# Performance work log

Measured on AMD Instinct MI355X. Metric: run time of the kernel, lower is better.

The kernel has to match this reference:

```python
import jax, jax.numpy as jnp
import numpy as np

SLOPE = 25.0   # fast_sigmoid surrogate slope
THR = 1.0      # snntorch Leaky default threshold


@jax.custom_vjp
def spike(x):
    # Heaviside forward, fast-sigmoid surrogate backward
    return (x > 0).astype(x.dtype)

def _spike_fwd(x):
    return spike(x), x

def _spike_bwd(x, g):
    return (g / (SLOPE * jnp.abs(x) + 1.0) ** 2,)

spike.defvjp(_spike_fwd, _spike_bwd)


def conv2d(x, w, b):
    y = jax.lax.conv_general_dilated(
        x, w, window_strides=(1, 1), padding=((1, 1), (1, 1)),
        dimension_numbers=('NCHW', 'OIHW', 'NCHW'))
    return y + b[None, :, None, None]


def maxpool2(x):
    return jax.lax.reduce_window(x, -jnp.inf, jax.lax.max,
                                 (1, 1, 2, 2), (1, 1, 2, 2), 'VALID')


def bn_inf(x, g, b, m, v):
    # inference-mode BatchNorm2d, eps = 1e-5
    inv = g * jax.lax.rsqrt(v + 1e-5)
    return x * inv[None, :, None, None] + (b - m * inv)[None, :, None, None]


def lif_step(mem, inp, beta):
    # snntorch Leaky, reset_mechanism='subtract', learn_beta (clamped to [0,1])
    b = jnp.clip(beta, 0.0, 1.0)
    reset = jax.lax.stop_gradient((mem > THR).astype(mem.dtype))
    mem_new = b * mem + inp - reset * THR
    spk = spike(mem_new - THR)
    return spk, mem_new


def setup_inputs() -> dict:
    key = jax.random.key(0)
    ks = jax.random.split(key, 20)
    T, B, H, W = 25, 512, 100, 64   # T steps, batch, MAX_LEN, N_MELS
    NUM_CLASSES = 35
    FLAT = 32 * (H // 4) * (W // 4)  # 12800
    f32 = jnp.float32
    inp = {
        'x': jax.random.normal(ks[0], (T, B, H, W), f32),
        'conv1_w': jax.random.normal(ks[1], (16, 1, 3, 3), f32) * 0.2,
        'conv1_b': jnp.zeros((16,), f32),
        'bn1_g': jnp.ones((16,), f32),
        'bn1_b': jnp.zeros((16,), f32),
        'bn1_m': jax.random.normal(ks[2], (16,), f32) * 0.1,
        'bn1_v': jax.random.uniform(ks[3], (16,), f32) + 0.5,
        'conv2_w': jax.random.normal(ks[4], (32, 16, 3, 3), f32) * (1.0 / np.sqrt(16 * 9)),
        'conv2_b': jnp.zeros((32,), f32),
        'bn2_g': jnp.ones((32,), f32),
        'bn2_b': jnp.zeros((32,), f32),
        'bn2_m': jax.random.normal(ks[5], (32,), f32) * 0.1,
        'bn2_v': jax.random.uniform(ks[6], (32,), f32) + 0.5,
        'fc1_w': jax.random.normal(ks[7], (256, FLAT), f32) * (1.0 / np.sqrt(FLAT)),
        'fc1_b': jnp.zeros((256,), f32),
        'fc2_w': jax.random.normal(ks[8], (128, 256), f32) * (1.0 / np.sqrt(256)),
        'fc2_b': jnp.zeros((128,), f32),
        'fc3_w': jax.random.normal(ks[9], (NUM_CLASSES, 128), f32) * (1.0 / np.sqrt(128)),
        'fc3_b': jnp.zeros((NUM_CLASSES,), f32),
        'beta1': jnp.float32(0.9),
        'beta2': jnp.float32(0.9),
        'beta3': jnp.float32(0.9),
    }
    return inp


def reference(x, conv1_w, conv1_b, bn1_g, bn1_b, bn1_m, bn1_v,
              conv2_w, conv2_b, bn2_g, bn2_b, bn2_m, bn2_v,
              fc1_w, fc1_b, fc2_w, fc2_b, fc3_w, fc3_b,
              beta1, beta2, beta3):
    T, B = x.shape[0], x.shape[1]
    # CNN runs once on the time-averaged input
    x_mean = jnp.mean(x, axis=0)[:, None]          # (B, 1, H, W)
    f = maxpool2(jax.nn.relu(bn_inf(conv2d(x_mean, conv1_w, conv1_b), bn1_g, bn1_b, bn1_m, bn1_v)))
    f = maxpool2(jax.nn.relu(bn_inf(conv2d(f, conv2_w, conv2_b), bn2_g, bn2_b, bn2_m, bn2_v)))
    feat = f.reshape(B, -1)                        # (B, FLAT)
    # fc1 input is the same every step (dropout = identity in eval)
    cur1 = feat @ fc1_w.T + fc1_b                  # (B, 256)

    m1 = jnp.zeros((B, fc1_w.shape[0]), x.dtype)
    m2 = jnp.zeros((B, fc2_w.shape[0]), x.dtype)
    m3 = jnp.zeros((B, fc3_w.shape[0]), x.dtype)

    def step(carry, _):
        m1, m2, m3 = carry
        spk1, m1 = lif_step(m1, cur1, beta1)
        spk2, m2 = lif_step(m2, spk1 @ fc2_w.T + fc2_b, beta2)
        spk3, m3 = lif_step(m3, spk2 @ fc3_w.T + fc3_b, beta3)
        return (m1, m2, m3), spk3

    _, out = jax.lax.scan(step, (m1, m2, m3), None, length=T)
    return out                                     # (T, B, NUM_CLASSES)
```

## Files before the change

### kernel.cpp

```cpp
#include <hip/hip_runtime.h>

typedef float f4nt __attribute__((ext_vector_type(4)));

#define WS_P1    0
#define WS_FEAT  13107200
#define WS_PART  0
#define WS_S1    8388608
#define WS_IN2   11665408
#define WS_S2    13303808
#define WS_IN3   14942208
#define WS_WL    19660800
#define WS_SH2   (WS_WL + 4608)

__global__ void prep_kernel(const float* __restrict__ w2, const float* __restrict__ cb2,
                            const float* __restrict__ g2, const float* __restrict__ bb2,
                            const float* __restrict__ m2, const float* __restrict__ v2,
                            float* __restrict__ wlg, float* __restrict__ sh2g) {
    const int tid = threadIdx.x;
    for (int i = tid; i < 4608; i += 256) {
        int c = i / 144, rem = i - c * 144;
        float inv = g2[c] * rsqrtf(v2[c] + 1e-5f);
        wlg[rem * 32 + c] = w2[i] * inv;
    }
    if (tid < 32) {
        float inv = g2[tid] * rsqrtf(v2[tid] + 1e-5f);
        sh2g[tid] = cb2[tid] * inv + bb2[tid] - m2[tid] * inv;
    }
}

__global__ __launch_bounds__(384) void conv1_kernel(const float* __restrict__ x,
                                                    const float* __restrict__ w1,
                                                    const float* __restrict__ cb1,
                                                    const float* __restrict__ g1,
                                                    const float* __restrict__ bb1,
                                                    const float* __restrict__ m1g,
                                                    const float* __restrict__ v1,
                                                    float* __restrict__ p1) {
    __shared__ float xs[22 * 66];
    __shared__ float w1s[144];
    __shared__ float sh1s[16];
    const int b = blockIdx.x, s = blockIdx.y;
    const int tid = threadIdx.x;
    if (tid < 144) {
        int c = tid / 9;
        float inv = g1[c] * rsqrtf(v1[c] + 1e-5f);
        w1s[tid] = w1[tid] * inv;
    }
    if (tid >= 144 && tid < 160) {
        int c = tid - 144;
        float inv = g1[c] * rsqrtf(v1[c] + 1e-5f);
        sh1s[c] = cb1[c] * inv + bb1[c] - m1g[c] * inv;
    }
    if (tid >= 160 && tid < 204) {
        int q = tid - 160;
        xs[(q >> 1) * 66 + (q & 1) * 65] = 0.f;
    }
    const int r0 = s * 20 - 1;
    const size_t TSTR = (size_t)512 * 6400;
    if (tid < 352) {
        int lr = tid >> 4, cq = tid & 15;
        int gr = r0 + lr;
        f4nt a0 = {0.f, 0.f, 0.f, 0.f}, a1 = a0, a2 = a0, a3 = a0;
        if (gr >= 0 && gr < 100) {
            const float* px = x + (size_t)b * 6400 + gr * 64 + cq * 4;
            #pragma unroll
            for (int tt = 0; tt < 24; tt += 4) {
                f4nt v0 = __builtin_nontemporal_load((const f4nt*)(px + (size_t)(tt + 0) * TSTR));
                f4nt v1_ = __builtin_nontemporal_load((const f4nt*)(px + (size_t)(tt + 1) * TSTR));
                f4nt v2_ = __builtin_nontemporal_load((const f4nt*)(px + (size_t)(tt + 2) * TSTR));
                f4nt v3 = __builtin_nontemporal_load((const f4nt*)(px + (size_t)(tt + 3) * TSTR));
                a0 += v0; a1 += v1_; a2 += v2_; a3 += v3;
            }
            f4nt v = __builtin_nontemporal_load((const f4nt*)(px + (size_t)24 * TSTR));
            a0 += v;
        }
        const float sc = 1.0f / 25.0f;
        f4nt sm = (a0 + a1 + a2 + a3) * sc;
        float* d = &xs[lr * 66 + 1 + cq * 4];
        d[0] = sm.x; d[1] = sm.y; d[2] = sm.z; d[3] = sm.w;
    }
    __syncthreads();
    if (tid < 320) {
        int phl = tid >> 5, pw = tid & 31;
        int ph = s * 10 + phl;
        float win[4][4];
        #pragma unroll
        for (int a = 0; a < 4; ++a)
            #pragma unroll
            for (int c2 = 0; c2 < 4; ++c2)
                win[a][c2] = xs[(2 * phl + a) * 66 + 2 * pw + c2];
        #pragma unroll 1
        for (int c = 0; c < 16; ++c) {
            float s00 = 0.f, s01 = 0.f, s10 = 0.f, s11 = 0.f;
            #pragma unroll
            for (int dh = 0; dh < 3; ++dh)
                #pragma unroll
                for (int dw = 0; dw < 3; ++dw) {
                    float w = w1s[c * 9 + dh * 3 + dw];
                    s00 = fmaf(win[dh][dw],         w, s00);
                    s01 = fmaf(win[dh][dw + 1],     w, s01);
                    s10 = fmaf(win[dh + 1][dw],     w, s10);
                    s11 = fmaf(win[dh + 1][dw + 1], w, s11);
                }
            float m = fmaxf(fmaxf(s00, s01), fmaxf(s10, s11));
            float val = fmaxf(m + sh1s[c], 0.f);
            p1[(((size_t)b * 50 + ph) * 16 + c) * 32 + pw] = val;
        }
    }
}

__global__ __launch_bounds__(256) void conv2_kernel(const float* __restrict__ p1,
                                                    const float* __restrict__ wlg,
                                                    const float* __restrict__ sh2g,
                                                    float* __restrict__ feat) {
    __shared__ __align__(16) float ins[10 * 16 * 36];
    const int s = blockIdx.x, b = blockIdx.y;
    const int tid = threadIdx.x;
    const int chg = tid & 15, q = (tid >> 4) & 3, phl = tid >> 6;
    const int ph = s * 4 + phl;
    const int xb = q * 8;
    const float* wbase = wlg + 2 * chg;

    float2 wcur[9], wnxt[9];
    #pragma unroll
    for (int t = 0; t < 9; ++t)
        wcur[t] = *(const float2*)&wbase[t * 32];
    if (tid < 160) {
        int lr = tid >> 4, ci = tid & 15;
        int gr = s * 8 - 1 + lr;
        float* dst = &ins[(lr * 16 + ci) * 36];
        if (gr >= 0 && gr < 50) {
            const float* src = p1 + (((size_t)b * 50 + gr) * 16 + ci) * 32;
            float4 v0 = *(const float4*)src;
            dst[0] = 0.f; dst[1] = v0.x; dst[2] = v0.y; dst[3] = v0.z;
            #pragma unroll
            for (int qq = 1; qq < 8; ++qq) {
                float4 v = *(const float4*)(src + 4 * qq - 1);
                *(float4*)(dst + 4 * qq) = v;
            }
            dst[32] = src[31];
            dst[33] = 0.f; dst[34] = 0.f; dst[35] = 0.f;
        } else {
            #pragma unroll
            for (int qq = 0; qq < 9; ++qq) *(float4*)(dst + 4 * qq) = make_float4(0.f, 0.f, 0.f, 0.f);
        }
    }
    __syncthreads();

    float acc[2][2][8];
    #pragma unroll
    for (int c = 0; c < 2; ++c)
        #pragma unroll
        for (int a = 0; a < 2; ++a)
            #pragma unroll
            for (int xx = 0; xx < 8; ++xx) acc[c][a][xx] = 0.f;

    #pragma unroll 1
    for (int ci = 0; ci < 16; ++ci) {
        if (ci < 15) {
            #pragma unroll
            for (int t = 0; t < 9; ++t)
                wnxt[t] = *(const float2*)&wbase[((ci + 1) * 9 + t) * 32];
        }
        #pragma unroll
        for (int lr4 = 0; lr4 < 4; ++lr4) {
            const float* row = &ins[((2 * phl + lr4) * 16 + ci) * 36 + xb];
            float v[10];
            float4 t0 = *(const float4*)&row[0];
            float4 t1 = *(const float4*)&row[4];
            float2 t2 = *(const float2*)&row[8];
            v[0]=t0.x; v[1]=t0.y; v[2]=t0.z; v[3]=t0.w;
            v[4]=t1.x; v[5]=t1.y; v[6]=t1.z; v[7]=t1.w;
            v[8]=t2.x; v[9]=t2.y;
            #pragma unroll
            for (int a = 0; a < 2; ++a) {
                const int dh = lr4 - a;
                if (dh >= 0 && dh <= 2) {
                    #pragma unroll
                    for (int dw = 0; dw < 3; ++dw) {
                        float w0 = wcur[dh * 3 + dw].x;
                        float w1 = wcur[dh * 3 + dw].y;
                        #pragma unroll
                        for (int xx = 0; xx < 8; ++xx) {
                            acc[0][a][xx] = fmaf(v[xx + dw], w0, acc[0][a][xx]);
                            acc[1][a][xx] = fmaf(v[xx + dw], w1, acc[1][a][xx]);
                        }
                    }
                }
            }
        }
        #pragma unroll
        for (int t = 0; t < 9; ++t) wcur[t] = wnxt[t];
    }
    if (ph < 25) {
        #pragma unroll
        for (int ch = 0; ch < 2; ++ch) {
            const int c = 2 * chg + ch;
            const float sh = sh2g[c];
            #pragma unroll
            for (int p = 0; p < 4; ++p) {
                float m = fmaxf(fmaxf(acc[ch][0][2 * p], acc[ch][0][2 * p + 1]),
                                fmaxf(acc[ch][1][2 * p], acc[ch][1][2 * p + 1]));
                float val = fmaxf(m + sh, 0.f);
                feat[(((size_t)b * 32 + c) * 25 + ph) * 16 + q * 4 + p] = val;
            }
        }
    }
}

__global__ __launch_bounds__(256, 1) void fc1_kernel(const float* __restrict__ feat,
                                                     const float* __restrict__ w,
                                                     float* __restrict__ part) {
    __shared__ float As[8 * 136];
    __shared__ float Bs[8 * 320];
    const int bx = blockIdx.x, bz = blockIdx.y;
    const int tid = threadIdx.x;
    const int tm = tid >> 5, tn = tid & 31;
    const int m0 = bx * 128;
    const int k0 = bz * 200;
    const int ar = tid >> 1, ac4 = (tid & 1) * 4;
    const int br = tid >> 1, bh = (tid & 1) * 4;
    const int gb0 = (br >> 3) * 10 + (br & 7);
    const int gb1 = ((br + 128) >> 3) * 10 + (br & 7);

    float acc[16][8] = {};
    float4 aP  = *(const float4*)(feat + (size_t)(m0 + ar) * 12800 + k0 + ac4);
    float4 bP0 = *(const float4*)(w + (size_t)br * 12800 + k0 + bh);
    float4 bP1 = *(const float4*)(w + (size_t)(br + 128) * 12800 + k0 + bh);

    for (int st = 0; st < 25; ++st) {
        __syncthreads();
        As[(ac4 + 0) * 136 + ar] = aP.x; As[(ac4 + 1) * 136 + ar] = aP.y;
        As[(ac4 + 2) * 136 + ar] = aP.z; As[(ac4 + 3) * 136 + ar] = aP.w;
        Bs[(bh + 0) * 320 + gb0] = bP0.x; Bs[(bh + 1) * 320 + gb0] = bP0.y;
        Bs[(bh + 2) * 320 + gb0] = bP0.z; Bs[(bh + 3) * 320 + gb0] = bP0.w;
        Bs[(bh + 0) * 320 + gb1] = bP1.x; Bs[(bh + 1) * 320 + gb1] = bP1.y;
        Bs[(bh + 2) * 320 + gb1] = bP1.z; Bs[(bh + 3) * 320 + gb1] = bP1.w;
        __syncthreads();
        if (st < 24) {
            const int o = k0 + (st + 1) * 8;
            aP  = *(const float4*)(feat + (size_t)(m0 + ar) * 12800 + o + ac4);
            bP0 = *(const float4*)(w + (size_t)br * 12800 + o + bh);
            bP1 = *(const float4*)(w + (size_t)(br + 128) * 12800 + o + bh);
        }
        #pragma unroll
        for (int kk = 0; kk < 8; ++kk) {
            float4 a0 = *(const float4*)&As[kk * 136 + tm * 16];
            float4 a1 = *(const float4*)&As[kk * 136 + tm * 16 + 4];
            float4 a2 = *(const float4*)&As[kk * 136 + tm * 16 + 8];
            float4 a3 = *(const float4*)&As[kk * 136 + tm * 16 + 12];
            float4 b0 = *(const float4*)&Bs[kk * 320 + tn * 10];
            float4 b1 = *(const float4*)&Bs[kk * 320 + tn * 10 + 4];
            float a_[16] = {a0.x, a0.y, a0.z, a0.w, a1.x, a1.y, a1.z, a1.w,
                            a2.x, a2.y, a2.z, a2.w, a3.x, a3.y, a3.z, a3.w};
            float b_[8]  = {b0.x, b0.y, b0.z, b0.w, b1.x, b1.y, b1.z, b1.w};
            #pragma unroll
            for (int i = 0; i < 16; ++i)
                #pragma unroll
                for (int j = 0; j < 8; ++j)
                    acc[i][j] = fmaf(a_[i], b_[j], acc[i][j]);
        }
    }
    #pragma unroll
    for (int i = 0; i < 16; ++i) {
        float* dst = &part[(size_t)bz * 131072 + (size_t)(m0 + tm * 16 + i) * 256 + tn * 8];
        *(float4*)dst       = make_float4(acc[i][0], acc[i][1], acc[i][2], acc[i][3]);
        *(float4*)(dst + 4) = make_float4(acc[i][4], acc[i][5], acc[i][6], acc[i][7]);
    }
}

__global__ __launch_bounds__(256) void lif1_kernel(const float* __restrict__ part,
                                                   const float* __restrict__ b1g,
                                                   const float* __restrict__ pb1,
                                                   float* __restrict__ S1) {
    const int i = blockIdx.x * 256 + threadIdx.x;
    const int k = i & 255;
    float cu = b1g[k];
    #pragma unroll 8
    for (int z = 0; z < 64; ++z) cu += part[(size_t)z * 131072 + i];
    const float be = fminf(fmaxf(pb1[0], 0.f), 1.f);
    float m = 0.f;
    #pragma unroll
    for (int t = 0; t < 25; ++t) {
        float r = (m > 1.f) ? 1.f : 0.f;
        m = fmaf(be, m, cu) - r;
        S1[(size_t)t * 131072 + i] = (m > 1.f) ? 1.f : 0.f;
    }
}

__global__ __launch_bounds__(256) void fc2g_kernel(const float* __restrict__ S1,
                                                   const float* __restrict__ w2g,
                                                   const float* __restrict__ b2g,
                                                   float* __restrict__ in2) {
    __shared__ float As[16 * 36];
    __shared__ float Bs[16 * 136];
    const int m0 = blockIdx.x * 32;
    const int tid = threadIdx.x;
    const int tm = tid >> 4, tn = tid & 15;
    const int ra = tid >> 2, cqa = tid & 3;
    const int rb = tid >> 1, kb = (tid & 1) * 8;
    float acc[2][8] = {};
    float4 av = make_float4(0.f, 0.f, 0.f, 0.f);
    if (tid < 128) av = *(const float4*)&S1[(size_t)(m0 + ra) * 256 + cqa * 4];
    float4 bv0 = *(const float4*)&w2g[rb * 256 + kb];
    float4 bv1 = *(const float4*)&w2g[rb * 256 + kb + 4];

    for (int kt = 0; kt < 16; ++kt) {
        __syncthreads();
        if (tid < 128) {
            As[(cqa * 4 + 0) * 36 + ra] = av.x; As[(cqa * 4 + 1) * 36 + ra] = av.y;
            As[(cqa * 4 + 2) * 36 + ra] = av.z; As[(cqa * 4 + 3) * 36 + ra] = av.w;
        }
        Bs[(kb + 0) * 136 + rb] = bv0.x; Bs[(kb + 1) * 136 + rb] = bv0.y;
        Bs[(kb + 2) * 136 + rb] = bv0.z; Bs[(kb + 3) * 136 + rb] = bv0.w;
        Bs[(kb + 4) * 136 + rb] = bv1.x; Bs[(kb + 5) * 136 + rb] = bv1.y;
        Bs[(kb + 6) * 136 + rb] = bv1.z; Bs[(kb + 7) * 136 + rb] = bv1.w;
        __syncthreads();
        if (kt < 15) {
            const int o = (kt + 1) * 16;
            if (tid < 128) av = *(const float4*)&S1[(size_t)(m0 + ra) * 256 + o + cqa * 4];
            bv0 = *(const float4*)&w2g[rb * 256 + o + kb];
            bv1 = *(const float4*)&w2g[rb * 256 + o + kb + 4];
        }
        #pragma unroll
        for (int kk = 0; kk < 16; ++kk) {
            float2 a2 = *(const float2*)&As[kk * 36 + tm * 2];
            float4 bw0 = *(const float4*)&Bs[kk * 136 + tn * 8];
            float4 bw1 = *(const float4*)&Bs[kk * 136 + tn * 8 + 4];
            float b_[8] = {bw0.x, bw0.y, bw0.z, bw0.w, bw1.x, bw1.y, bw1.z, bw1.w};
            #pragma unroll
            for (int j = 0; j < 8; ++j) {
                acc[0][j] = fmaf(a2.x, b_[j], acc[0][j]);
                acc[1][j] = fmaf(a2.y, b_[j], acc[1][j]);
            }
        }
    }
    float4 bb0 = *(const float4*)&b2g[tn * 8];
    float4 bb1 = *(const float4*)&b2g[tn * 8 + 4];
    #pragma unroll
    for (int i = 0; i < 2; ++i) {
        float* dst = &in2[(size_t)(m0 + tm * 2 + i) * 128 + tn * 8];
        *(float4*)dst       = make_float4(acc[i][0] + bb0.x, acc[i][1] + bb0.y,
                                          acc[i][2] + bb0.z, acc[i][3] + bb0.w);
        *(float4*)(dst + 4) = make_float4(acc[i][4] + bb1.x, acc[i][5] + bb1.y,
                                          acc[i][6] + bb1.z, acc[i][7] + bb1.w);
    }
}

__global__ __launch_bounds__(256) void lif2_kernel(const float* __restrict__ in2,
                                                   const float* __restrict__ pb2,
                                                   float* __restrict__ S2) {
    const int i = blockIdx.x * 256 + threadIdx.x;
    const float be = fminf(fmaxf(pb2[0], 0.f), 1.f);
    float m = 0.f;
    #pragma unroll
    for (int t = 0; t < 25; ++t) {
        float r = (m > 1.f) ? 1.f : 0.f;
        m = fmaf(be, m, in2[(size_t)t * 65536 + i]) - r;
        S2[(size_t)t * 65536 + i] = (m > 1.f) ? 1.f : 0.f;
    }
}

__global__ __launch_bounds__(256) void fc3g_kernel(const float* __restrict__ S2,
                                                   const float* __restrict__ w3g,
                                                   const float* __restrict__ b3g,
                                                   float* __restrict__ in3) {
    __shared__ float As[16 * 36];
    __shared__ float Bs[16 * 48];
    const int m0 = blockIdx.x * 32;
    const int tid = threadIdx.x;
    const int tm = tid >> 4, tn = tid & 15;
    float acc[2][3] = {};
    for (int kt = 0; kt < 8; ++kt) {
        __syncthreads();
        if (tid < 128) {
            int r = tid >> 2, cq = tid & 3;
            float4 av = *(const float4*)&S2[(size_t)(m0 + r) * 128 + kt * 16 + cq * 4];
            As[(cq * 4 + 0) * 36 + r] = av.x; As[(cq * 4 + 1) * 36 + r] = av.y;
            As[(cq * 4 + 2) * 36 + r] = av.z; As[(cq * 4 + 3) * 36 + r] = av.w;
        }
        for (int i = tid; i < 560; i += 256) {
            int kk = i / 35, c = i - kk * 35;
            Bs[kk * 48 + c] = w3g[c * 128 + kt * 16 + kk];
        }
        __syncthreads();
        #pragma unroll
        for (int kk = 0; kk < 16; ++kk) {
            float2 a2 = *(const float2*)&As[kk * 36 + tm * 2];
            float w0 = Bs[kk * 48 + tn];
            float w1 = Bs[kk * 48 + tn + 16];
            float w2 = Bs[kk * 48 + tn + 32];
            acc[0][0] = fmaf(a2.x, w0, acc[0][0]); acc[1][0] = fmaf(a2.y, w0, acc[1][0]);
            acc[0][1] = fmaf(a2.x, w1, acc[0][1]); acc[1][1] = fmaf(a2.y, w1, acc[1][1]);
            acc[0][2] = fmaf(a2.x, w2, acc[0][2]); acc[1][2] = fmaf(a2.y, w2, acc[1][2]);
        }
    }
    const float bias0 = b3g[tn];
    const float bias1 = b3g[tn + 16];
    const float bias2 = (tn < 3) ? b3g[tn + 32] : 0.f;
    #pragma unroll
    for (int i = 0; i < 2; ++i) {
        const size_t row = (size_t)(m0 + tm * 2 + i) * 35;
        in3[row + tn]      = acc[i][0] + bias0;
        in3[row + tn + 16] = acc[i][1] + bias1;
        if (tn < 3) in3[row + tn + 32] = acc[i][2] + bias2;
    }
}

__global__ __launch_bounds__(256) void lif3_kernel(const float* __restrict__ in3,
                                                   const float* __restrict__ pb3,
                                                   float* __restrict__ out) {
    const int i = blockIdx.x * 256 + threadIdx.x;
    if (i >= 17920) return;
    const float be = fminf(fmaxf(pb3[0], 0.f), 1.f);
    float m = 0.f;
    #pragma unroll
    for (int t = 0; t < 25; ++t) {
        float r = (m > 1.f) ? 1.f : 0.f;
        m = fmaf(be, m, in3[(size_t)t * 17920 + i]) - r;
        out[(size_t)t * 17920 + i] = (m > 1.f) ? 1.f : 0.f;
    }
}

extern "C" void kernel_launch(void* const* d_in, const int* in_sizes, int n_in,
                              void* d_out, int out_size, void* d_ws, size_t ws_size,
                              hipStream_t stream) {
    const float* x     = (const float*)d_in[0];
    const float* c1w   = (const float*)d_in[1];
    const float* c1b   = (const float*)d_in[2];
    const float* bn1g  = (const float*)d_in[3];
    const float* bn1b  = (const float*)d_in[4];
    const float* bn1m  = (const float*)d_in[5];
    const float* bn1v  = (const float*)d_in[6];
    const float* c2w   = (const float*)d_in[7];
    const float* c2b   = (const float*)d_in[8];
    const float* bn2g  = (const float*)d_in[9];
    const float* bn2b  = (const float*)d_in[10];
    const float* bn2m  = (const float*)d_in[11];
    const float* bn2v  = (const float*)d_in[12];
    const float* fc1w  = (const float*)d_in[13];
    const float* fc1b  = (const float*)d_in[14];
    const float* fc2w  = (const float*)d_in[15];
    const float* fc2b  = (const float*)d_in[16];
    const float* fc3w  = (const float*)d_in[17];
    const float* fc3b  = (const float*)d_in[18];
    const float* beta1 = (const float*)d_in[19];
    const float* beta2 = (const float*)d_in[20];
    const float* beta3 = (const float*)d_in[21];
    float* ws  = (float*)d_ws;
    float* out = (float*)d_out;

    prep_kernel<<<1, 256, 0, stream>>>(c2w, c2b, bn2g, bn2b, bn2m, bn2v,
                                       ws + WS_WL, ws + WS_SH2);
    conv1_kernel<<<dim3(512, 5), 384, 0, stream>>>(x, c1w, c1b, bn1g, bn1b, bn1m, bn1v,
                                                   ws + WS_P1);
    conv2_kernel<<<dim3(7, 512), 256, 0, stream>>>(ws + WS_P1, ws + WS_WL, ws + WS_SH2,
                                                   ws + WS_FEAT);
    fc1_kernel<<<dim3(4, 64), 256, 0, stream>>>(ws + WS_FEAT, fc1w, ws + WS_PART);
    lif1_kernel<<<512, 256, 0, stream>>>(ws + WS_PART, fc1b, beta1, ws + WS_S1);
    fc2g_kernel<<<400, 256, 0, stream>>>(ws + WS_S1, fc2w, fc2b, ws + WS_IN2);
    lif2_kernel<<<256, 256, 0, stream>>>(ws + WS_IN2, beta2, ws + WS_S2);
    fc3g_kernel<<<400, 256, 0, stream>>>(ws + WS_S2, fc3w, fc3b, ws + WS_IN3);
    lif3_kernel<<<70, 256, 0, stream>>>(ws + WS_IN3, beta3, out);
}
```

Measured before the change: 299.3 us.

## Fuse conv1 and conv2 into one kernel keeping pooled conv1 output in LDS

Merges the conv1+BN+ReLU+pool stage with the conv2 stage so the intermediate pooled map stays in shared memory instead of going through global memory. Each block now recomputes conv1 for its halo rows, reading 22 input rows across all 25 timesteps per 8-row output tile. This removes the intermediate write/read and one launch, but increases redundant reads of the large time-series input due to halo overlap.

```diff
diff --git a/kernel.cpp b/kernel.cpp
--- a/kernel.cpp
+++ b/kernel.cpp
@@ -2,7 +2,6 @@
 
 typedef float f4nt __attribute__((ext_vector_type(4)));
 
-#define WS_P1    0
 #define WS_FEAT  13107200
 #define WS_PART  0
 #define WS_S1    8388608
@@ -28,19 +27,23 @@
     }
 }
 
-__global__ __launch_bounds__(384) void conv1_kernel(const float* __restrict__ x,
-                                                    const float* __restrict__ w1,
-                                                    const float* __restrict__ cb1,
-                                                    const float* __restrict__ g1,
-                                                    const float* __restrict__ bb1,
-                                                    const float* __restrict__ m1g,
-                                                    const float* __restrict__ v1,
-                                                    float* __restrict__ p1) {
+__global__ __launch_bounds__(256) void fused_conv_kernel(const float* __restrict__ x,
+                                                         const float* __restrict__ w1,
+                                                         const float* __restrict__ cb1,
+                                                         const float* __restrict__ g1,
+                                                         const float* __restrict__ bb1,
+                                                         const float* __restrict__ m1g,
+                                                         const float* __restrict__ v1,
+                                                         const float* __restrict__ wlg,
+                                                         const float* __restrict__ sh2g,
+                                                         float* __restrict__ feat) {
     __shared__ float xs[22 * 66];
+    __shared__ __align__(16) float p1L[10 * 16 * 36];
     __shared__ float w1s[144];
     __shared__ float sh1s[16];
-    const int b = blockIdx.x, s = blockIdx.y;
+    const int s = blockIdx.x, b = blockIdx.y;
     const int tid = threadIdx.x;
+
     if (tid < 144) {
         int c = tid / 9;
         float inv = g1[c] * rsqrtf(v1[c] + 1e-5f);
@@ -51,102 +54,84 @@
         float inv = g1[c] * rsqrtf(v1[c] + 1e-5f);
         sh1s[c] = cb1[c] * inv + bb1[c] - m1g[c] * inv;
     }
-    if (tid >= 160 && tid < 204) {
-        int q = tid - 160;
+
+    const size_t TSTR = (size_t)512 * 6400;
+    if (tid < 176) {
+        int lr = tid >> 3, cq = tid & 7;
+        int gxr = 16 * s - 3 + lr;
+        f4nt a0 = {0.f, 0.f, 0.f, 0.f}, a1 = a0, c0 = a0, c1 = a0;
+        if (gxr >= 0 && gxr < 100) {
+            const float* px = x + (size_t)b * 6400 + gxr * 64 + cq * 8;
+            #pragma unroll
+            for (int tt = 0; tt < 24; tt += 2) {
+                f4nt u0 = __builtin_nontemporal_load((const f4nt*)(px + (size_t)tt * TSTR));
+                f4nt u1 = __builtin_nontemporal_load((const f4nt*)(px + (size_t)tt * TSTR + 4));
+                f4nt u2 = __builtin_nontemporal_load((const f4nt*)(px + (size_t)(tt + 1) * TSTR));
+                f4nt u3 = __builtin_nontemporal_load((const f4nt*)(px + (size_t)(tt + 1) * TSTR + 4));
+                a0 += u0; a1 += u1; c0 += u2; c1 += u3;
+            }
+            f4nt u0 = __builtin_nontemporal_load((const f4nt*)(px + (size_t)24 * TSTR));
+            f4nt u1 = __builtin_nontemporal_load((const f4nt*)(px + (size_t)24 * TSTR + 4));
+            a0 += u0; a1 += u1;
+            a0 += c0; a1 += c1;
+            a0 *= (1.0f / 25.0f); a1 *= (1.0f / 25.0f);
+        }
+        float* d = &xs[lr * 66 + 1 + cq * 8];
+        d[0] = a0.x; d[1] = a0.y; d[2] = a0.z; d[3] = a0.w;
+        d[4] = a1.x; d[5] = a1.y; d[6] = a1.z; d[7] = a1.w;
+    } else if (tid < 220) {
+        int q = tid - 176;
         xs[(q >> 1) * 66 + (q & 1) * 65] = 0.f;
     }
-    const int r0 = s * 20 - 1;
-    const size_t TSTR = (size_t)512 * 6400;
-    if (tid < 352) {
-        int lr = tid >> 4, cq = tid & 15;
-        int gr = r0 + lr;
-        f4nt a0 = {0.f, 0.f, 0.f, 0.f}, a1 = a0, a2 = a0, a3 = a0;
-        if (gr >= 0 && gr < 100) {
-            const float* px = x + (size_t)b * 6400 + gr * 64 + cq * 4;
-            #pragma unroll
-            for (int tt = 0; tt < 24; tt += 4) {
-                f4nt v0 = __builtin_nontemporal_load((const f4nt*)(px + (size_t)(tt + 0) * TSTR));
-                f4nt v1_ = __builtin_nontemporal_load((const f4nt*)(px + (size_t)(tt + 1) * TSTR));
-                f4nt v2_ = __builtin_nontemporal_load((const f4nt*)(px + (size_t)(tt + 2) * TSTR));
-                f4nt v3 = __builtin_nontemporal_load((const f4nt*)(px + (size_t)(tt + 3) * TSTR));
-                a0 += v0; a1 += v1_; a2 += v2_; a3 += v3;
+    __syncthreads();
+
+    #pragma unroll 1
+    for (int pos = tid; pos < 320; pos += 256) {
+        int j = pos >> 5, pw = pos & 31;
+        int gr = s * 8 - 1 + j;
+        if (gr >= 0 && gr < 50) {
+            float win[4][4];
+            #pragma unroll
+            for (int a = 0; a < 4; ++a)
+                #pragma unroll
+                for (int cc = 0; cc < 4; ++cc)
+                    win[a][cc] = xs[(2 * j + a) * 66 + 2 * pw + cc];
+            #pragma unroll 1
+            for (int c = 0; c < 16; ++c) {
+                float s00 = 0.f, s01 = 0.f, s10 = 0.f, s11 = 0.f;
+                #pragma unroll
+                for (int dh = 0; dh < 3; ++dh)
+                    #pragma unroll
+                    for (int dw = 0; dw < 3; ++dw) {
+                        float w = w1s[c * 9 + dh * 3 + dw];
+                        s00 = fmaf(win[dh][dw],         w, s00);
+                        s01 = fmaf(win[dh][dw + 1],     w, s01);
+                        s10 = fmaf(win[dh + 1][dw],     w, s10);
+                        s11 = fmaf(win[dh + 1][dw + 1], w, s11);
+                    }
+                float m = fmaxf(fmaxf(s00, s01), fmaxf(s10, s11));
+                p1L[(j * 16 + c) * 36 + 1 + pw] = fmaxf(m + sh1s[c], 0.f);
             }
-            f4nt v = __builtin_nontemporal_load((const f4nt*)(px + (size_t)24 * TSTR));
-            a0 += v;
-        }
-        const float sc = 1.0f / 25.0f;
-        f4nt sm = (a0 + a1 + a2 + a3) * sc;
-        float* d = &xs[lr * 66 + 1 + cq * 4];
-        d[0] = sm.x; d[1] = sm.y; d[2] = sm.z; d[3] = sm.w;
-    }
-    __syncthreads();
-    if (tid < 320) {
-        int phl = tid >> 5, pw = tid & 31;
-        int ph = s * 10 + phl;
-        float win[4][4];
-        #pragma unroll
-        for (int a = 0; a < 4; ++a)
-            #pragma unroll
-            for (int c2 = 0; c2 < 4; ++c2)
-                win[a][c2] = xs[(2 * phl + a) * 66 + 2 * pw + c2];
-        #pragma unroll 1
-        for (int c = 0; c < 16; ++c) {
-            float s00 = 0.f, s01 = 0.f, s10 = 0.f, s11 = 0.f;
-            #pragma unroll
-            for (int dh = 0; dh < 3; ++dh)
-                #pragma unroll
-                for (int dw = 0; dw < 3; ++dw) {
-                    float w = w1s[c * 9 + dh * 3 + dw];
-                    s00 = fmaf(win[dh][dw],         w, s00);
-                    s01 = fmaf(win[dh][dw + 1],     w, s01);
-                    s10 = fmaf(win[dh + 1][dw],     w, s10);
-                    s11 = fmaf(win[dh + 1][dw + 1], w, s11);
-                }
-            float m = fmaxf(fmaxf(s00, s01), fmaxf(s10, s11));
-            float val = fmaxf(m + sh1s[c], 0.f);
-            p1[(((size_t)b * 50 + ph) * 16 + c) * 32 + pw] = val;
-        }
-    }
-}
-
-__global__ __launch_bounds__(256) void conv2_kernel(const float* __restrict__ p1,
-                                                    const float* __restrict__ wlg,
-                                                    const float* __restrict__ sh2g,
-                                                    float* __restrict__ feat) {
-    __shared__ __align__(16) float ins[10 * 16 * 36];
-    const int s = blockIdx.x, b = blockIdx.y;
-    const int tid = threadIdx.x;
-    const int chg = tid & 15, q = (tid >> 4) & 3, phl = tid >> 6;
-    const int ph = s * 4 + phl;
-    const int xb = q * 8;
+        } else {
+            #pragma unroll
+            for (int c = 0; c < 16; ++c)
+                p1L[(j * 16 + c) * 36 + 1 + pw] = 0.f;
+        }
+    }
+    const int chg = tid & 15, q2 = (tid >> 4) & 3, phl = tid >> 6;
     const float* wbase = wlg + 2 * chg;
-
     float2 wcur[9], wnxt[9];
     #pragma unroll
     for (int t = 0; t < 9; ++t)
         wcur[t] = *(const float2*)&wbase[t * 32];
-    if (tid < 160) {
-        int lr = tid >> 4, ci = tid & 15;
-        int gr = s * 8 - 1 + lr;
-        float* dst = &ins[(lr * 16 + ci) * 36];
-        if (gr >= 0 && gr < 50) {
-            const float* src = p1 + (((size_t)b * 50 + gr) * 16 + ci) * 32;
-            float4 v0 = *(const float4*)src;
-            dst[0] = 0.f; dst[1] = v0.x; dst[2] = v0.y; dst[3] = v0.z;
-            #pragma unroll
-            for (int qq = 1; qq < 8; ++qq) {
-                float4 v = *(const float4*)(src + 4 * qq - 1);
-                *(float4*)(dst + 4 * qq) = v;
-            }
-            dst[32] = src[31];
-            dst[33] = 0.f; dst[34] = 0.f; dst[35] = 0.f;
-        } else {
-            #pragma unroll
-            for (int qq = 0; qq < 9; ++qq) *(float4*)(dst + 4 * qq) = make_float4(0.f, 0.f, 0.f, 0.f);
-        }
+    for (int i = tid; i < 640; i += 256) {
+        int rowi = i >> 2, col = i & 3;
+        p1L[rowi * 36 + (col == 0 ? 0 : 32 + col)] = 0.f;
     }
     __syncthreads();
 
+    const int ph = s * 4 + phl;
+    const int xb = q2 * 8;
     float acc[2][2][8];
     #pragma unroll
     for (int c = 0; c < 2; ++c)
@@ -164,7 +149,7 @@
         }
         #pragma unroll
         for (int lr4 = 0; lr4 < 4; ++lr4) {
-            const float* row = &ins[((2 * phl + lr4) * 16 + ci) * 36 + xb];
+            const float* row = &p1L[((2 * phl + lr4) * 16 + ci) * 36 + xb];
             float v[10];
             float4 t0 = *(const float4*)&row[0];
             float4 t1 = *(const float4*)&row[4];
@@ -202,7 +187,7 @@
                 float m = fmaxf(fmaxf(acc[ch][0][2 * p], acc[ch][0][2 * p + 1]),
                                 fmaxf(acc[ch][1][2 * p], acc[ch][1][2 * p + 1]));
                 float val = fmaxf(m + sh, 0.f);
-                feat[(((size_t)b * 32 + c) * 25 + ph) * 16 + q * 4 + p] = val;
+                feat[(((size_t)b * 32 + c) * 25 + ph) * 16 + q2 * 4 + p] = val;
             }
         }
     }
@@ -452,10 +437,8 @@
 
     prep_kernel<<<1, 256, 0, stream>>>(c2w, c2b, bn2g, bn2b, bn2m, bn2v,
                                        ws + WS_WL, ws + WS_SH2);
-    conv1_kernel<<<dim3(512, 5), 384, 0, stream>>>(x, c1w, c1b, bn1g, bn1b, bn1m, bn1v,
-                                                   ws + WS_P1);
-    conv2_kernel<<<dim3(7, 512), 256, 0, stream>>>(ws + WS_P1, ws + WS_WL, ws + WS_SH2,
-                                                   ws + WS_FEAT);
+    fused_conv_kernel<<<dim3(7, 512), 256, 0, stream>>>(x, c1w, c1b, bn1g, bn1b, bn1m, bn1v,
+                                                        ws + WS_WL, ws + WS_SH2, ws + WS_FEAT);
     fc1_kernel<<<dim3(4, 64), 256, 0, stream>>>(ws + WS_FEAT, fc1w, ws + WS_PART);
     lif1_kernel<<<512, 256, 0, stream>>>(ws + WS_PART, fc1b, beta1, ws + WS_S1);
     fc2g_kernel<<<400, 256, 0, stream>>>(ws + WS_S1, fc2w, fc2b, ws + WS_IN2);
```

Result: faster. 281.7 us, median of 2 (-5.9%).
